# Optimization experiments

Hardware: AMD Instinct MI355X
Metric: run time of the kernel (lower is better)

## Reference

```python
import jax, jax.numpy as jnp
import numpy as np

B, N = 8192, 200  # batch of patches, fixed 200 points per patch


def setup_inputs() -> dict:
    key = jax.random.key(0)
    k1, = jax.random.split(key, 1)
    network_in = jax.random.normal(k1, (B, N, 13), dtype=jnp.float32)
    # learned parameters per build(): outward_shift init 0.25, a init 1, b init 0
    outward_shift = jnp.full((1,), 0.25, dtype=jnp.float32)
    a = jnp.ones((1,), dtype=jnp.float32)
    b = jnp.zeros((1,), dtype=jnp.float32)
    return {"network_in": network_in, "outward_shift": outward_shift, "a": a, "b": b}


def reference(network_in, outward_shift, a, b):
    w = network_in[:, :, 0:1]          # [B,N,1]
    xyz1 = network_in[:, :, 1:4]
    xyz2 = network_in[:, :, 4:7]       # also orig_xyz2
    norm1 = network_in[:, :, 7:10]
    norm2 = network_in[:, :, 10:13]

    w = jax.nn.relu(a * w + b) + 1e-8  # [B,N,1]

    v1 = xyz1 + norm1 * outward_shift
    v2 = xyz2 + norm2 * outward_shift

    w_sum = jnp.sum(w, axis=1)                       # [B,1]
    v1_ctr = jnp.sum(v1 * w, axis=1) / w_sum         # [B,3]
    v2_ctr = jnp.sum(v2 * w, axis=1) / w_sum         # [B,3]
    v1 = v1 - v1_ctr[:, None, :]
    v2 = v2 - v2_ctr[:, None, :]

    # cov = v2^T diag(w) v1, done without materializing the NxN diagonal
    cov = jnp.einsum('bni,bn,bnj->bij', v2, w[:, :, 0], v1)  # [B,3,3]

    # tf.linalg.svd: cov = u diag(s) v^T  ->  jnp svd: cov = u diag(s) vh, v = vh^T
    u, s, vh = jnp.linalg.svd(cov)
    v = jnp.swapaxes(vh, -1, -2)

    VUt = jnp.einsum('bik,bjk->bij', v, u)           # v @ u^T
    det_VUt = jnp.linalg.det(VUt)                    # [B]
    ones = jnp.ones_like(det_VUt)
    d = jnp.stack([ones, ones, det_VUt], axis=-1)    # [B,3]

    # R = v @ diag([1,1,det]) @ u^T
    R = jnp.einsum('bik,bk,bjk->bij', v, d, u)       # [B,3,3]

    t = v1_ctr - jnp.einsum('bij,bj->bi', R, v2_ctr) # [B,3]
    new_coords = jnp.einsum('bij,bnj->bni', R, xyz2) + t[:, None, :]
    return new_coords
```

## Files before the change

### kernel.cpp

```cpp
#include <hip/hip_runtime.h>
#include <math.h>

#define NPTS 200
#define NCH  13
#define BLK  256
#define FPB  (NPTS * NCH)
#define STG  2560

typedef float f4u __attribute__((ext_vector_type(4), aligned(4)));

typedef struct { float x, y, z; } f3s;

#define ACCUMULATE(Q0,Q1,Q2,Q3,Q4,Q5,Q6,Q7,Q8,Q9,Q10,Q11,Q12)               \
    {                                                                        \
        float wt = aa * (Q0) + bb;                                           \
        wt = fmaxf(wt, 0.f) + 1e-8f;                                         \
        const float v1x = fmaf(shift, (Q7),  (Q1));                          \
        const float v1y = fmaf(shift, (Q8),  (Q2));                          \
        const float v1z = fmaf(shift, (Q9),  (Q3));                          \
        const float v2x = fmaf(shift, (Q10), (Q4));                          \
        const float v2y = fmaf(shift, (Q11), (Q5));                          \
        const float v2z = fmaf(shift, (Q12), (Q6));                          \
        const float wv2x = wt * v2x, wv2y = wt * v2y, wv2z = wt * v2z;       \
        acc[0] += wt;                                                        \
        acc[1] += wt * v1x; acc[2] += wt * v1y; acc[3] += wt * v1z;          \
        acc[4] += wv2x;     acc[5] += wv2y;     acc[6] += wv2z;              \
        acc[7]  += wv2x * v1x; acc[8]  += wv2x * v1y; acc[9]  += wv2x * v1z; \
        acc[10] += wv2y * v1x; acc[11] += wv2y * v1y; acc[12] += wv2y * v1z; \
        acc[13] += wv2z * v1x; acc[14] += wv2z * v1y; acc[15] += wv2z * v1z; \
    }

__global__ __launch_bounds__(BLK, 4) void fused_kernel(
    const float* __restrict__ net_in,
    const float* __restrict__ shift_p,
    const float* __restrict__ a_p,
    const float* __restrict__ b_p,
    float* __restrict__ out)
{
    __shared__ float s_in[4 * STG];

    const int tid = threadIdx.x;
    const int w   = tid >> 6;
    const int l   = tid & 63;
    const int b   = blockIdx.x * 4 + w;

    const float shift = shift_p[0];
    const float aa    = a_p[0];
    const float bb    = b_p[0];

    const float* src = net_in + (size_t)b * FPB;
    float*       dst = s_in + w * STG;

    #pragma unroll
    for (int j = 0; j < 10; ++j) {
        __builtin_amdgcn_global_load_lds(
            (const __attribute__((address_space(1))) void*)(src + j * 256 + l * 4),
            (__attribute__((address_space(3))) void*)(dst + j * 256),
            16, 0, 0);
    }

    f4u t0v = {0.f, 0.f, 0.f, 0.f};
    f4u t1v = {0.f, 0.f, 0.f, 0.f};
    f4u t2v = {0.f, 0.f, 0.f, 0.f};
    float t12 = 0.f;
    if (l < 8) {
        const float* tp = src + (192 + l) * NCH;
        t0v = *(const f4u*)(tp);
        t1v = *(const f4u*)(tp + 4);
        t2v = *(const f4u*)(tp + 8);
        t12 = tp[12];
    }

    __builtin_amdgcn_s_waitcnt(0);
    __asm__ __volatile__("" ::: "memory");

    float acc[16];
    #pragma unroll
    for (int k = 0; k < 16; ++k) acc[k] = 0.f;

    float sx2[4], sy2[4], sz2[4];

    #pragma unroll
    for (int j = 0; j < 3; ++j) {
        const int p = l + 64 * j;
        const float* q = dst + p * NCH;
        const float q0 = q[0],  q1 = q[1],  q2  = q[2],  q3  = q[3];
        const float q4 = q[4],  q5 = q[5],  q6  = q[6],  q7  = q[7];
        const float q8 = q[8],  q9 = q[9],  q10 = q[10], q11 = q[11], q12 = q[12];
        ACCUMULATE(q0, q1, q2, q3, q4, q5, q6, q7, q8, q9, q10, q11, q12)
        sx2[j] = q4; sy2[j] = q5; sz2[j] = q6;
    }
    sx2[3] = t1v.x; sy2[3] = t1v.y; sz2[3] = t1v.z;
    if (l < 8) {
        ACCUMULATE(t0v.x, t0v.y, t0v.z, t0v.w,
                   t1v.x, t1v.y, t1v.z, t1v.w,
                   t2v.x, t2v.y, t2v.z, t2v.w, t12)
    }

    #pragma unroll
    for (int k = 0; k < 16; ++k) {
        acc[k] += __shfl_xor(acc[k], 32, 64);
        acc[k] += __shfl_xor(acc[k], 16, 64);
        acc[k] += __shfl_xor(acc[k],  8, 64);
        acc[k] += __shfl_xor(acc[k],  4, 64);
        acc[k] += __shfl_xor(acc[k],  2, 64);
        acc[k] += __shfl_xor(acc[k],  1, 64);
    }

    const float W = acc[0];
    const float invW = 1.0f / W;
    const float v1cx = acc[1] * invW, v1cy = acc[2] * invW, v1cz = acc[3] * invW;
    const float v2cx = acc[4] * invW, v2cy = acc[5] * invW, v2cz = acc[6] * invW;

    const float Sxx = acc[7]  - W * v2cx * v1cx;
    const float Sxy = acc[8]  - W * v2cx * v1cy;
    const float Sxz = acc[9]  - W * v2cx * v1cz;
    const float Syx = acc[10] - W * v2cy * v1cx;
    const float Syy = acc[11] - W * v2cy * v1cy;
    const float Syz = acc[12] - W * v2cy * v1cz;
    const float Szx = acc[13] - W * v2cz * v1cx;
    const float Szy = acc[14] - W * v2cz * v1cy;
    const float Szz = acc[15] - W * v2cz * v1cz;

    float Am[4][4];
    Am[0][0] = Sxx + Syy + Szz;
    Am[0][1] = Syz - Szy;  Am[0][2] = Szx - Sxz;  Am[0][3] = Sxy - Syx;
    Am[1][1] = Sxx - Syy - Szz;
    Am[1][2] = Sxy + Syx;  Am[1][3] = Szx + Sxz;
    Am[2][2] = -Sxx + Syy - Szz;
    Am[2][3] = Syz + Szy;
    Am[3][3] = -Sxx - Syy + Szz;
    Am[1][0] = Am[0][1]; Am[2][0] = Am[0][2]; Am[3][0] = Am[0][3];
    Am[2][1] = Am[1][2]; Am[3][1] = Am[1][3]; Am[3][2] = Am[2][3];

    float Vm[4][4] = {{1,0,0,0},{0,1,0,0},{0,0,1,0},{0,0,0,1}};

    const int prs[6][2] = {{0,1},{0,2},{0,3},{1,2},{1,3},{2,3}};
    for (int sweep = 0; sweep < 5; ++sweep) {
        #pragma unroll
        for (int r = 0; r < 6; ++r) {
            const int p = prs[r][0], q = prs[r][1];
            float apq = Am[p][q];
            if (apq != 0.0f) {
                float tau = (Am[q][q] - Am[p][p]) / (2.0f * apq);
                float t = copysignf(1.0f, tau) /
                          (fabsf(tau) + sqrtf(1.0f + tau * tau));
                float c = rsqrtf(1.0f + t * t);
                float s = t * c;
                #pragma unroll
                for (int k = 0; k < 4; ++k) {
                    float a1 = Am[p][k], a2 = Am[q][k];
                    Am[p][k] = c * a1 - s * a2;
                    Am[q][k] = s * a1 + c * a2;
                }
                #pragma unroll
                for (int k = 0; k < 4; ++k) {
                    float a1 = Am[k][p], a2 = Am[k][q];
                    Am[k][p] = c * a1 - s * a2;
                    Am[k][q] = s * a1 + c * a2;
                }
                #pragma unroll
                for (int k = 0; k < 4; ++k) {
                    float a1 = Vm[k][p], a2 = Vm[k][q];
                    Vm[k][p] = c * a1 - s * a2;
                    Vm[k][q] = s * a1 + c * a2;
                }
            }
        }
    }

    float bd = Am[0][0];
    float q0 = Vm[0][0], qx = Vm[1][0], qy = Vm[2][0], qz = Vm[3][0];
    if (Am[1][1] > bd) { bd = Am[1][1]; q0 = Vm[0][1]; qx = Vm[1][1]; qy = Vm[2][1]; qz = Vm[3][1]; }
    if (Am[2][2] > bd) { bd = Am[2][2]; q0 = Vm[0][2]; qx = Vm[1][2]; qy = Vm[2][2]; qz = Vm[3][2]; }
    if (Am[3][3] > bd) { bd = Am[3][3]; q0 = Vm[0][3]; qx = Vm[1][3]; qy = Vm[2][3]; qz = Vm[3][3]; }

    const float R00 = q0*q0 + qx*qx - qy*qy - qz*qz;
    const float R01 = 2.0f * (qx*qy - q0*qz);
    const float R02 = 2.0f * (qx*qz + q0*qy);
    const float R10 = 2.0f * (qx*qy + q0*qz);
    const float R11 = q0*q0 - qx*qx + qy*qy - qz*qz;
    const float R12 = 2.0f * (qy*qz - q0*qx);
    const float R20 = 2.0f * (qx*qz - q0*qy);
    const float R21 = 2.0f * (qy*qz + q0*qx);
    const float R22 = q0*q0 - qx*qx - qy*qy + qz*qz;

    const float tx = v1cx - (R00 * v2cx + R01 * v2cy + R02 * v2cz);
    const float ty = v1cy - (R10 * v2cx + R11 * v2cy + R12 * v2cz);
    const float tz = v1cz - (R20 * v2cx + R21 * v2cy + R22 * v2cz);

    float* ob = out + (size_t)b * (NPTS * 3);
    #pragma unroll
    for (int j = 0; j < 4; ++j) {
        if (j < 3 || l < 8) {
            const int p = l + 64 * j;
            const float X = sx2[j], Y = sy2[j], Z = sz2[j];
            f3s o3;
            o3.x = R00 * X + R01 * Y + R02 * Z + tx;
            o3.y = R10 * X + R11 * Y + R12 * Z + ty;
            o3.z = R20 * X + R21 * Y + R22 * Z + tz;
            *(f3s*)(ob + p * 3) = o3;
        }
    }
}

extern "C" void kernel_launch(void* const* d_in, const int* in_sizes, int n_in,
                              void* d_out, int out_size, void* d_ws, size_t ws_size,
                              hipStream_t stream) {
    const float* net_in  = (const float*)d_in[0];
    const float* shift_p = (const float*)d_in[1];
    const float* a_p     = (const float*)d_in[2];
    const float* b_p     = (const float*)d_in[3];
    float* out = (float*)d_out;

    const int B = in_sizes[0] / FPB;
    (void)d_ws; (void)ws_size; (void)n_in; (void)out_size;

    fused_kernel<<<B / 4, BLK, 0, stream>>>(net_in, shift_p, a_p, b_p, out);
}
```

Measured before the change: 162.5 us.

## Load points directly from global, reduce via LDS, solve eigenproblem in one thread per patch

Drops the global-to-LDS staging and reads each point's 13 channels straight from global memory with vector loads. The 16 accumulators are now reduced with two shuffles plus an LDS transpose-sum instead of six xor-shuffle rounds. The 4x4 Jacobi eigen solve runs in only 4 threads per block, one per patch, rather than redundantly in all 64 lanes, and it uses fast rcp/sqrt/rsq intrinsics plus quaternion renormalisation. Risks: uncoalesced 13-float-stride global loads, two block barriers, and a serial tail where only 4 lanes are active.

```diff
diff --git a/kernel.cpp b/kernel.cpp
--- a/kernel.cpp
+++ b/kernel.cpp
@@ -5,7 +5,6 @@
 #define NCH  13
 #define BLK  256
 #define FPB  (NPTS * NCH)
-#define STG  2560
 
 typedef float f4u __attribute__((ext_vector_type(4), aligned(4)));
 
@@ -37,7 +36,9 @@
     const float* __restrict__ b_p,
     float* __restrict__ out)
 {
-    __shared__ float s_in[4 * STG];
+    __shared__ float s_part[4][16][20];
+    __shared__ float s_sums[4][16];
+    __shared__ float s_Rt[4][12];
 
     const int tid = threadIdx.x;
     const int w   = tid >> 6;
@@ -49,30 +50,6 @@
     const float bb    = b_p[0];
 
     const float* src = net_in + (size_t)b * FPB;
-    float*       dst = s_in + w * STG;
-
-    #pragma unroll
-    for (int j = 0; j < 10; ++j) {
-        __builtin_amdgcn_global_load_lds(
-            (const __attribute__((address_space(1))) void*)(src + j * 256 + l * 4),
-            (__attribute__((address_space(3))) void*)(dst + j * 256),
-            16, 0, 0);
-    }
-
-    f4u t0v = {0.f, 0.f, 0.f, 0.f};
-    f4u t1v = {0.f, 0.f, 0.f, 0.f};
-    f4u t2v = {0.f, 0.f, 0.f, 0.f};
-    float t12 = 0.f;
-    if (l < 8) {
-        const float* tp = src + (192 + l) * NCH;
-        t0v = *(const f4u*)(tp);
-        t1v = *(const f4u*)(tp + 4);
-        t2v = *(const f4u*)(tp + 8);
-        t12 = tp[12];
-    }
-
-    __builtin_amdgcn_s_waitcnt(0);
-    __asm__ __volatile__("" ::: "memory");
 
     float acc[16];
     #pragma unroll
@@ -81,113 +58,142 @@
     float sx2[4], sy2[4], sz2[4];
 
     #pragma unroll
-    for (int j = 0; j < 3; ++j) {
-        const int p = l + 64 * j;
-        const float* q = dst + p * NCH;
-        const float q0 = q[0],  q1 = q[1],  q2  = q[2],  q3  = q[3];
-        const float q4 = q[4],  q5 = q[5],  q6  = q[6],  q7  = q[7];
-        const float q8 = q[8],  q9 = q[9],  q10 = q[10], q11 = q[11], q12 = q[12];
-        ACCUMULATE(q0, q1, q2, q3, q4, q5, q6, q7, q8, q9, q10, q11, q12)
-        sx2[j] = q4; sy2[j] = q5; sz2[j] = q6;
-    }
-    sx2[3] = t1v.x; sy2[3] = t1v.y; sz2[3] = t1v.z;
-    if (l < 8) {
-        ACCUMULATE(t0v.x, t0v.y, t0v.z, t0v.w,
-                   t1v.x, t1v.y, t1v.z, t1v.w,
-                   t2v.x, t2v.y, t2v.z, t2v.w, t12)
+    for (int j = 0; j < 4; ++j) {
+        if (j < 3 || l < 8) {
+            const float* q = src + (l + 64 * j) * NCH;
+            const f4u v0 = *(const f4u*)(q);
+            const f4u v1 = *(const f4u*)(q + 4);
+            const f4u v2 = *(const f4u*)(q + 8);
+            const float q12 = q[12];
+            ACCUMULATE(v0.x, v0.y, v0.z, v0.w,
+                       v1.x, v1.y, v1.z, v1.w,
+                       v2.x, v2.y, v2.z, v2.w, q12)
+            sx2[j] = v1.x; sy2[j] = v1.y; sz2[j] = v1.z;
+        } else {
+            sx2[j] = 0.f; sy2[j] = 0.f; sz2[j] = 0.f;
+        }
     }
 
     #pragma unroll
     for (int k = 0; k < 16; ++k) {
-        acc[k] += __shfl_xor(acc[k], 32, 64);
-        acc[k] += __shfl_xor(acc[k], 16, 64);
-        acc[k] += __shfl_xor(acc[k],  8, 64);
-        acc[k] += __shfl_xor(acc[k],  4, 64);
-        acc[k] += __shfl_xor(acc[k],  2, 64);
-        acc[k] += __shfl_xor(acc[k],  1, 64);
-    }
-
-    const float W = acc[0];
-    const float invW = 1.0f / W;
-    const float v1cx = acc[1] * invW, v1cy = acc[2] * invW, v1cz = acc[3] * invW;
-    const float v2cx = acc[4] * invW, v2cy = acc[5] * invW, v2cz = acc[6] * invW;
-
-    const float Sxx = acc[7]  - W * v2cx * v1cx;
-    const float Sxy = acc[8]  - W * v2cx * v1cy;
-    const float Sxz = acc[9]  - W * v2cx * v1cz;
-    const float Syx = acc[10] - W * v2cy * v1cx;
-    const float Syy = acc[11] - W * v2cy * v1cy;
-    const float Syz = acc[12] - W * v2cy * v1cz;
-    const float Szx = acc[13] - W * v2cz * v1cx;
-    const float Szy = acc[14] - W * v2cz * v1cy;
-    const float Szz = acc[15] - W * v2cz * v1cz;
-
-    float Am[4][4];
-    Am[0][0] = Sxx + Syy + Szz;
-    Am[0][1] = Syz - Szy;  Am[0][2] = Szx - Sxz;  Am[0][3] = Sxy - Syx;
-    Am[1][1] = Sxx - Syy - Szz;
-    Am[1][2] = Sxy + Syx;  Am[1][3] = Szx + Sxz;
-    Am[2][2] = -Sxx + Syy - Szz;
-    Am[2][3] = Syz + Szy;
-    Am[3][3] = -Sxx - Syy + Szz;
-    Am[1][0] = Am[0][1]; Am[2][0] = Am[0][2]; Am[3][0] = Am[0][3];
-    Am[2][1] = Am[1][2]; Am[3][1] = Am[1][3]; Am[3][2] = Am[2][3];
-
-    float Vm[4][4] = {{1,0,0,0},{0,1,0,0},{0,0,1,0},{0,0,0,1}};
-
-    const int prs[6][2] = {{0,1},{0,2},{0,3},{1,2},{1,3},{2,3}};
-    for (int sweep = 0; sweep < 5; ++sweep) {
+        acc[k] += __shfl_down(acc[k], 32, 64);
+        acc[k] += __shfl_down(acc[k], 16, 64);
+    }
+    if (l < 16) {
+        float4* pp = (float4*)&s_part[w][l][0];
+        pp[0] = make_float4(acc[0],  acc[1],  acc[2],  acc[3]);
+        pp[1] = make_float4(acc[4],  acc[5],  acc[6],  acc[7]);
+        pp[2] = make_float4(acc[8],  acc[9],  acc[10], acc[11]);
+        pp[3] = make_float4(acc[12], acc[13], acc[14], acc[15]);
+        float s = 0.f;
         #pragma unroll
-        for (int r = 0; r < 6; ++r) {
-            const int p = prs[r][0], q = prs[r][1];
-            float apq = Am[p][q];
-            if (apq != 0.0f) {
-                float tau = (Am[q][q] - Am[p][p]) / (2.0f * apq);
-                float t = copysignf(1.0f, tau) /
-                          (fabsf(tau) + sqrtf(1.0f + tau * tau));
-                float c = rsqrtf(1.0f + t * t);
-                float s = t * c;
-                #pragma unroll
-                for (int k = 0; k < 4; ++k) {
-                    float a1 = Am[p][k], a2 = Am[q][k];
-                    Am[p][k] = c * a1 - s * a2;
-                    Am[q][k] = s * a1 + c * a2;
-                }
-                #pragma unroll
-                for (int k = 0; k < 4; ++k) {
-                    float a1 = Am[k][p], a2 = Am[k][q];
-                    Am[k][p] = c * a1 - s * a2;
-                    Am[k][q] = s * a1 + c * a2;
-                }
-                #pragma unroll
-                for (int k = 0; k < 4; ++k) {
-                    float a1 = Vm[k][p], a2 = Vm[k][q];
-                    Vm[k][p] = c * a1 - s * a2;
-                    Vm[k][q] = s * a1 + c * a2;
+        for (int r = 0; r < 16; ++r) s += s_part[w][r][l];
+        s_sums[w][l] = s;
+    }
+    __syncthreads();
+
+    if (tid < 4) {
+        float f[16];
+        #pragma unroll
+        for (int k = 0; k < 16; ++k) f[k] = s_sums[tid][k];
+
+        const float W = f[0];
+        const float invW = __builtin_amdgcn_rcpf(W);
+        const float v1cx = f[1] * invW, v1cy = f[2] * invW, v1cz = f[3] * invW;
+        const float v2cx = f[4] * invW, v2cy = f[5] * invW, v2cz = f[6] * invW;
+
+        const float Sxx = f[7]  - W * v2cx * v1cx;
+        const float Sxy = f[8]  - W * v2cx * v1cy;
+        const float Sxz = f[9]  - W * v2cx * v1cz;
+        const float Syx = f[10] - W * v2cy * v1cx;
+        const float Syy = f[11] - W * v2cy * v1cy;
+        const float Syz = f[12] - W * v2cy * v1cz;
+        const float Szx = f[13] - W * v2cz * v1cx;
+        const float Szy = f[14] - W * v2cz * v1cy;
+        const float Szz = f[15] - W * v2cz * v1cz;
+
+        float Am[4][4];
+        Am[0][0] = Sxx + Syy + Szz;
+        Am[0][1] = Syz - Szy;  Am[0][2] = Szx - Sxz;  Am[0][3] = Sxy - Syx;
+        Am[1][1] = Sxx - Syy - Szz;
+        Am[1][2] = Sxy + Syx;  Am[1][3] = Szx + Sxz;
+        Am[2][2] = -Sxx + Syy - Szz;
+        Am[2][3] = Syz + Szy;
+        Am[3][3] = -Sxx - Syy + Szz;
+        Am[1][0] = Am[0][1]; Am[2][0] = Am[0][2]; Am[3][0] = Am[0][3];
+        Am[2][1] = Am[1][2]; Am[3][1] = Am[1][3]; Am[3][2] = Am[2][3];
+
+        float Vm[4][4] = {{1,0,0,0},{0,1,0,0},{0,0,1,0},{0,0,0,1}};
+
+        const int prs[6][2] = {{0,1},{0,2},{0,3},{1,2},{1,3},{2,3}};
+        for (int sweep = 0; sweep < 5; ++sweep) {
+            #pragma unroll
+            for (int r = 0; r < 6; ++r) {
+                const int p = prs[r][0], q = prs[r][1];
+                float apq = Am[p][q];
+                if (apq != 0.0f) {
+                    float tau = (Am[q][q] - Am[p][p]) * 0.5f *
+                                __builtin_amdgcn_rcpf(apq);
+                    float t = copysignf(1.0f, tau) * __builtin_amdgcn_rcpf(
+                                fabsf(tau) +
+                                __builtin_amdgcn_sqrtf(fmaf(tau, tau, 1.0f)));
+                    float c = __builtin_amdgcn_rsqf(fmaf(t, t, 1.0f));
+                    float s = t * c;
+                    #pragma unroll
+                    for (int k = 0; k < 4; ++k) {
+                        float a1 = Am[p][k], a2 = Am[q][k];
+                        Am[p][k] = c * a1 - s * a2;
+                        Am[q][k] = s * a1 + c * a2;
+                    }
+                    #pragma unroll
+                    for (int k = 0; k < 4; ++k) {
+                        float a1 = Am[k][p], a2 = Am[k][q];
+                        Am[k][p] = c * a1 - s * a2;
+                        Am[k][q] = s * a1 + c * a2;
+                    }
+                    #pragma unroll
+                    for (int k = 0; k < 4; ++k) {
+                        float a1 = Vm[k][p], a2 = Vm[k][q];
+                        Vm[k][p] = c * a1 - s * a2;
+                        Vm[k][q] = s * a1 + c * a2;
+                    }
                 }
             }
         }
-    }
-
-    float bd = Am[0][0];
-    float q0 = Vm[0][0], qx = Vm[1][0], qy = Vm[2][0], qz = Vm[3][0];
-    if (Am[1][1] > bd) { bd = Am[1][1]; q0 = Vm[0][1]; qx = Vm[1][1]; qy = Vm[2][1]; qz = Vm[3][1]; }
-    if (Am[2][2] > bd) { bd = Am[2][2]; q0 = Vm[0][2]; qx = Vm[1][2]; qy = Vm[2][2]; qz = Vm[3][2]; }
-    if (Am[3][3] > bd) { bd = Am[3][3]; q0 = Vm[0][3]; qx = Vm[1][3]; qy = Vm[2][3]; qz = Vm[3][3]; }
-
-    const float R00 = q0*q0 + qx*qx - qy*qy - qz*qz;
-    const float R01 = 2.0f * (qx*qy - q0*qz);
-    const float R02 = 2.0f * (qx*qz + q0*qy);
-    const float R10 = 2.0f * (qx*qy + q0*qz);
-    const float R11 = q0*q0 - qx*qx + qy*qy - qz*qz;
-    const float R12 = 2.0f * (qy*qz - q0*qx);
-    const float R20 = 2.0f * (qx*qz - q0*qy);
-    const float R21 = 2.0f * (qy*qz + q0*qx);
-    const float R22 = q0*q0 - qx*qx - qy*qy + qz*qz;
-
-    const float tx = v1cx - (R00 * v2cx + R01 * v2cy + R02 * v2cz);
-    const float ty = v1cy - (R10 * v2cx + R11 * v2cy + R12 * v2cz);
-    const float tz = v1cz - (R20 * v2cx + R21 * v2cy + R22 * v2cz);
+
+        float bd = Am[0][0];
+        float q0 = Vm[0][0], qx = Vm[1][0], qy = Vm[2][0], qz = Vm[3][0];
+        if (Am[1][1] > bd) { bd = Am[1][1]; q0 = Vm[0][1]; qx = Vm[1][1]; qy = Vm[2][1]; qz = Vm[3][1]; }
+        if (Am[2][2] > bd) { bd = Am[2][2]; q0 = Vm[0][2]; qx = Vm[1][2]; qy = Vm[2][2]; qz = Vm[3][2]; }
+        if (Am[3][3] > bd) { bd = Am[3][3]; q0 = Vm[0][3]; qx = Vm[1][3]; qy = Vm[2][3]; qz = Vm[3][3]; }
+
+        const float qn = __builtin_amdgcn_rsqf(q0*q0 + qx*qx + qy*qy + qz*qz);
+        q0 *= qn; qx *= qn; qy *= qn; qz *= qn;
+
+        const float R00 = q0*q0 + qx*qx - qy*qy - qz*qz;
+        const float R01 = 2.0f * (qx*qy - q0*qz);
+        const float R02 = 2.0f * (qx*qz + q0*qy);
+        const float R10 = 2.0f * (qx*qy + q0*qz);
+        const float R11 = q0*q0 - qx*qx + qy*qy - qz*qz;
+        const float R12 = 2.0f * (qy*qz - q0*qx);
+        const float R20 = 2.0f * (qx*qz - q0*qy);
+        const float R21 = 2.0f * (qy*qz + q0*qx);
+        const float R22 = q0*q0 - qx*qx - qy*qy + qz*qz;
+
+        float* o = &s_Rt[tid][0];
+        o[0] = R00; o[1]  = R01; o[2]  = R02;
+        o[3] = R10; o[4]  = R11; o[5]  = R12;
+        o[6] = R20; o[7]  = R21; o[8]  = R22;
+        o[9]  = v1cx - (R00 * v2cx + R01 * v2cy + R02 * v2cz);
+        o[10] = v1cy - (R10 * v2cx + R11 * v2cy + R12 * v2cz);
+        o[11] = v1cz - (R20 * v2cx + R21 * v2cy + R22 * v2cz);
+    }
+    __syncthreads();
+
+    const float R00 = s_Rt[w][0], R01 = s_Rt[w][1],  R02 = s_Rt[w][2];
+    const float R10 = s_Rt[w][3], R11 = s_Rt[w][4],  R12 = s_Rt[w][5];
+    const float R20 = s_Rt[w][6], R21 = s_Rt[w][7],  R22 = s_Rt[w][8];
+    const float tx  = s_Rt[w][9], ty  = s_Rt[w][10], tz  = s_Rt[w][11];
 
     float* ob = out + (size_t)b * (NPTS * 3);
     #pragma unroll
```

Result: faster. 144.4 us (-11.2%).

## Load patch points directly from global memory and use fast hardware reciprocals

Applied to the files above, without the earlier changes.

Drops the LDS staging buffer and its async global-to-LDS copies. Each lane now reads its 13 channels straight from global memory with unaligned float4 loads, which removes the shared-memory footprint and the full waitcnt barrier. The Jacobi rotations and centroid division switch to raw hardware rcp, sqrt and rsq builtins in place of IEEE division. The quaternion is renormalised to compensate for the lower precision. The risk is uncoalesced strided global loads (13-float stride per lane) in exchange for removing LDS traffic and raising occupancy.

```diff
diff --git a/kernel.cpp b/kernel.cpp
--- a/kernel.cpp
+++ b/kernel.cpp
@@ -5,7 +5,6 @@
 #define NCH  13
 #define BLK  256
 #define FPB  (NPTS * NCH)
-#define STG  2560
 
 typedef float f4u __attribute__((ext_vector_type(4), aligned(4)));
 
@@ -37,8 +36,6 @@
     const float* __restrict__ b_p,
     float* __restrict__ out)
 {
-    __shared__ float s_in[4 * STG];
-
     const int tid = threadIdx.x;
     const int w   = tid >> 6;
     const int l   = tid & 63;
@@ -49,30 +46,6 @@
     const float bb    = b_p[0];
 
     const float* src = net_in + (size_t)b * FPB;
-    float*       dst = s_in + w * STG;
-
-    #pragma unroll
-    for (int j = 0; j < 10; ++j) {
-        __builtin_amdgcn_global_load_lds(
-            (const __attribute__((address_space(1))) void*)(src + j * 256 + l * 4),
-            (__attribute__((address_space(3))) void*)(dst + j * 256),
-            16, 0, 0);
-    }
-
-    f4u t0v = {0.f, 0.f, 0.f, 0.f};
-    f4u t1v = {0.f, 0.f, 0.f, 0.f};
-    f4u t2v = {0.f, 0.f, 0.f, 0.f};
-    float t12 = 0.f;
-    if (l < 8) {
-        const float* tp = src + (192 + l) * NCH;
-        t0v = *(const f4u*)(tp);
-        t1v = *(const f4u*)(tp + 4);
-        t2v = *(const f4u*)(tp + 8);
-        t12 = tp[12];
-    }
-
-    __builtin_amdgcn_s_waitcnt(0);
-    __asm__ __volatile__("" ::: "memory");
 
     float acc[16];
     #pragma unroll
@@ -81,20 +54,20 @@
     float sx2[4], sy2[4], sz2[4];
 
     #pragma unroll
-    for (int j = 0; j < 3; ++j) {
-        const int p = l + 64 * j;
-        const float* q = dst + p * NCH;
-        const float q0 = q[0],  q1 = q[1],  q2  = q[2],  q3  = q[3];
-        const float q4 = q[4],  q5 = q[5],  q6  = q[6],  q7  = q[7];
-        const float q8 = q[8],  q9 = q[9],  q10 = q[10], q11 = q[11], q12 = q[12];
-        ACCUMULATE(q0, q1, q2, q3, q4, q5, q6, q7, q8, q9, q10, q11, q12)
-        sx2[j] = q4; sy2[j] = q5; sz2[j] = q6;
-    }
-    sx2[3] = t1v.x; sy2[3] = t1v.y; sz2[3] = t1v.z;
-    if (l < 8) {
-        ACCUMULATE(t0v.x, t0v.y, t0v.z, t0v.w,
-                   t1v.x, t1v.y, t1v.z, t1v.w,
-                   t2v.x, t2v.y, t2v.z, t2v.w, t12)
+    for (int j = 0; j < 4; ++j) {
+        if (j < 3 || l < 8) {
+            const float* q = src + (l + 64 * j) * NCH;
+            const f4u v0 = *(const f4u*)(q);
+            const f4u v1 = *(const f4u*)(q + 4);
+            const f4u v2 = *(const f4u*)(q + 8);
+            const float q12 = q[12];
+            ACCUMULATE(v0.x, v0.y, v0.z, v0.w,
+                       v1.x, v1.y, v1.z, v1.w,
+                       v2.x, v2.y, v2.z, v2.w, q12)
+            sx2[j] = v1.x; sy2[j] = v1.y; sz2[j] = v1.z;
+        } else {
+            sx2[j] = 0.f; sy2[j] = 0.f; sz2[j] = 0.f;
+        }
     }
 
     #pragma unroll
@@ -108,7 +81,7 @@
     }
 
     const float W = acc[0];
-    const float invW = 1.0f / W;
+    const float invW = __builtin_amdgcn_rcpf(W);
     const float v1cx = acc[1] * invW, v1cy = acc[2] * invW, v1cz = acc[3] * invW;
     const float v2cx = acc[4] * invW, v2cy = acc[5] * invW, v2cz = acc[6] * invW;
 
@@ -142,10 +115,12 @@
             const int p = prs[r][0], q = prs[r][1];
             float apq = Am[p][q];
             if (apq != 0.0f) {
-                float tau = (Am[q][q] - Am[p][p]) / (2.0f * apq);
-                float t = copysignf(1.0f, tau) /
-                          (fabsf(tau) + sqrtf(1.0f + tau * tau));
-                float c = rsqrtf(1.0f + t * t);
+                float tau = (Am[q][q] - Am[p][p]) * 0.5f *
+                            __builtin_amdgcn_rcpf(apq);
+                float t = copysignf(1.0f, tau) * __builtin_amdgcn_rcpf(
+                            fabsf(tau) +
+                            __builtin_amdgcn_sqrtf(fmaf(tau, tau, 1.0f)));
+                float c = __builtin_amdgcn_rsqf(fmaf(t, t, 1.0f));
                 float s = t * c;
                 #pragma unroll
                 for (int k = 0; k < 4; ++k) {
@@ -174,6 +149,9 @@
     if (Am[1][1] > bd) { bd = Am[1][1]; q0 = Vm[0][1]; qx = Vm[1][1]; qy = Vm[2][1]; qz = Vm[3][1]; }
     if (Am[2][2] > bd) { bd = Am[2][2]; q0 = Vm[0][2]; qx = Vm[1][2]; qy = Vm[2][2]; qz = Vm[3][2]; }
     if (Am[3][3] > bd) { bd = Am[3][3]; q0 = Vm[0][3]; qx = Vm[1][3]; qy = Vm[2][3]; qz = Vm[3][3]; }
+
+    const float qn = __builtin_amdgcn_rsqf(q0*q0 + qx*qx + qy*qy + qz*qz);
+    q0 *= qn; qx *= qn; qy *= qn; qz *= qn;
 
     const float R00 = q0*q0 + qx*qx - qy*qy - qz*qz;
     const float R01 = 2.0f * (qx*qy - q0*qz);
```

Measured after the change: 154.4 us. 5.0% less time.

## Streamline 4x4 Jacobi eigensolver with scalar symmetric entries and fast intrinsics

Applied to the files above, without the earlier changes.

Replaces the full 4x4 array Jacobi rotation with a symmetric scalar form. Each rotation updates the two diagonal entries in closed form, zeroes the pivot, and rotates only the four affected off-diagonal entries. Divisions and square roots become hardware rcp/sqrt/rsq intrinsics, and the sweep count drops from five to four, with a quaternion renormalisation added afterwards. This cuts per-thread ALU work and register pressure in the serial eigen-solve tail, at the cost of lower-precision intrinsics and one fewer sweep, which could affect accuracy.

```diff
diff --git a/kernel.cpp b/kernel.cpp
--- a/kernel.cpp
+++ b/kernel.cpp
@@ -30,6 +30,32 @@
         acc[13] += wv2z * v1x; acc[14] += wv2z * v1y; acc[15] += wv2z * v1z; \
     }
 
+#define ROT(dp, dq, opq, e1p, e1q, e2p, e2q, P, Q)                           \
+    {                                                                        \
+        const float apq = opq;                                               \
+        if (apq != 0.0f) {                          \
+            const float tau = (dq - dp) * 0.5f * __builtin_amdgcn_rcpf(apq); \
+            const float tt  = copysignf(1.0f, tau) * __builtin_amdgcn_rcpf(  \
+                                fabsf(tau) +                                 \
+                                __builtin_amdgcn_sqrtf(fmaf(tau, tau, 1.0f)));\
+            const float c = __builtin_amdgcn_rsqf(fmaf(tt, tt, 1.0f));       \
+            const float s = tt * c;                                          \
+            dp -= tt * apq;                                                  \
+            dq += tt * apq;                                                  \
+            opq = 0.0f;                                                      \
+            { const float t1 = e1p; e1p = c * t1 - s * e1q;                  \
+              e1q = s * t1 + c * e1q; }                                      \
+            { const float t2 = e2p; e2p = c * t2 - s * e2q;                  \
+              e2q = s * t2 + c * e2q; }                                      \
+            _Pragma("unroll")                                                \
+            for (int k = 0; k < 4; ++k) {                                    \
+                const float a1 = Vm[k][P], a2 = Vm[k][Q];                    \
+                Vm[k][P] = c * a1 - s * a2;                                  \
+                Vm[k][Q] = s * a1 + c * a2;                                  \
+            }                                                                \
+        }                                                                    \
+    }
+
 __global__ __launch_bounds__(BLK, 4) void fused_kernel(
     const float* __restrict__ net_in,
     const float* __restrict__ shift_p,
@@ -52,10 +78,10 @@
     float*       dst = s_in + w * STG;
 
     #pragma unroll
-    for (int j = 0; j < 10; ++j) {
+    for (int jj = 0; jj < 10; ++jj) {
         __builtin_amdgcn_global_load_lds(
-            (const __attribute__((address_space(1))) void*)(src + j * 256 + l * 4),
-            (__attribute__((address_space(3))) void*)(dst + j * 256),
+            (const __attribute__((address_space(1))) void*)(src + jj * 256 + l * 4),
+            (__attribute__((address_space(3))) void*)(dst + jj * 256),
             16, 0, 0);
     }
 
@@ -81,14 +107,14 @@
     float sx2[4], sy2[4], sz2[4];
 
     #pragma unroll
-    for (int j = 0; j < 3; ++j) {
-        const int p = l + 64 * j;
+    for (int jj = 0; jj < 3; ++jj) {
+        const int p = l + 64 * jj;
         const float* q = dst + p * NCH;
         const float q0 = q[0],  q1 = q[1],  q2  = q[2],  q3  = q[3];
         const float q4 = q[4],  q5 = q[5],  q6  = q[6],  q7  = q[7];
         const float q8 = q[8],  q9 = q[9],  q10 = q[10], q11 = q[11], q12 = q[12];
         ACCUMULATE(q0, q1, q2, q3, q4, q5, q6, q7, q8, q9, q10, q11, q12)
-        sx2[j] = q4; sy2[j] = q5; sz2[j] = q6;
+        sx2[jj] = q4; sy2[jj] = q5; sz2[jj] = q6;
     }
     sx2[3] = t1v.x; sy2[3] = t1v.y; sz2[3] = t1v.z;
     if (l < 8) {
@@ -108,7 +134,7 @@
     }
 
     const float W = acc[0];
-    const float invW = 1.0f / W;
+    const float invW = __builtin_amdgcn_rcpf(W);
     const float v1cx = acc[1] * invW, v1cy = acc[2] * invW, v1cz = acc[3] * invW;
     const float v2cx = acc[4] * invW, v2cy = acc[5] * invW, v2cz = acc[6] * invW;
 
@@ -122,58 +148,36 @@
     const float Szy = acc[14] - W * v2cz * v1cy;
     const float Szz = acc[15] - W * v2cz * v1cz;
 
-    float Am[4][4];
-    Am[0][0] = Sxx + Syy + Szz;
-    Am[0][1] = Syz - Szy;  Am[0][2] = Szx - Sxz;  Am[0][3] = Sxy - Syx;
-    Am[1][1] = Sxx - Syy - Szz;
-    Am[1][2] = Sxy + Syx;  Am[1][3] = Szx + Sxz;
-    Am[2][2] = -Sxx + Syy - Szz;
-    Am[2][3] = Syz + Szy;
-    Am[3][3] = -Sxx - Syy + Szz;
-    Am[1][0] = Am[0][1]; Am[2][0] = Am[0][2]; Am[3][0] = Am[0][3];
-    Am[2][1] = Am[1][2]; Am[3][1] = Am[1][3]; Am[3][2] = Am[2][3];
+    float d0  = Sxx + Syy + Szz;
+    float o01 = Syz - Szy;
+    float o02 = Szx - Sxz;
+    float o03 = Sxy - Syx;
+    float d1  = Sxx - Syy - Szz;
+    float o12 = Sxy + Syx;
+    float o13 = Szx + Sxz;
+    float d2  = -Sxx + Syy - Szz;
+    float o23 = Syz + Szy;
+    float d3  = -Sxx - Syy + Szz;
 
     float Vm[4][4] = {{1,0,0,0},{0,1,0,0},{0,0,1,0},{0,0,0,1}};
 
-    const int prs[6][2] = {{0,1},{0,2},{0,3},{1,2},{1,3},{2,3}};
-    for (int sweep = 0; sweep < 5; ++sweep) {
-        #pragma unroll
-        for (int r = 0; r < 6; ++r) {
-            const int p = prs[r][0], q = prs[r][1];
-            float apq = Am[p][q];
-            if (apq != 0.0f) {
-                float tau = (Am[q][q] - Am[p][p]) / (2.0f * apq);
-                float t = copysignf(1.0f, tau) /
-                          (fabsf(tau) + sqrtf(1.0f + tau * tau));
-                float c = rsqrtf(1.0f + t * t);
-                float s = t * c;
-                #pragma unroll
-                for (int k = 0; k < 4; ++k) {
-                    float a1 = Am[p][k], a2 = Am[q][k];
-                    Am[p][k] = c * a1 - s * a2;
-                    Am[q][k] = s * a1 + c * a2;
-                }
-                #pragma unroll
-                for (int k = 0; k < 4; ++k) {
-                    float a1 = Am[k][p], a2 = Am[k][q];
-                    Am[k][p] = c * a1 - s * a2;
-                    Am[k][q] = s * a1 + c * a2;
-                }
-                #pragma unroll
-                for (int k = 0; k < 4; ++k) {
-                    float a1 = Vm[k][p], a2 = Vm[k][q];
-                    Vm[k][p] = c * a1 - s * a2;
-                    Vm[k][q] = s * a1 + c * a2;
-                }
-            }
-        }
-    }
-
-    float bd = Am[0][0];
+    for (int sweep = 0; sweep < 4; ++sweep) {
+        ROT(d0, d1, o01,  o02, o12,  o03, o13,  0, 1)
+        ROT(d0, d2, o02,  o01, o12,  o03, o23,  0, 2)
+        ROT(d0, d3, o03,  o01, o13,  o02, o23,  0, 3)
+        ROT(d1, d2, o12,  o01, o02,  o13, o23,  1, 2)
+        ROT(d1, d3, o13,  o01, o03,  o12, o23,  1, 3)
+        ROT(d2, d3, o23,  o02, o03,  o12, o13,  2, 3)
+    }
+
+    float bd = d0;
     float q0 = Vm[0][0], qx = Vm[1][0], qy = Vm[2][0], qz = Vm[3][0];
-    if (Am[1][1] > bd) { bd = Am[1][1]; q0 = Vm[0][1]; qx = Vm[1][1]; qy = Vm[2][1]; qz = Vm[3][1]; }
-    if (Am[2][2] > bd) { bd = Am[2][2]; q0 = Vm[0][2]; qx = Vm[1][2]; qy = Vm[2][2]; qz = Vm[3][2]; }
-    if (Am[3][3] > bd) { bd = Am[3][3]; q0 = Vm[0][3]; qx = Vm[1][3]; qy = Vm[2][3]; qz = Vm[3][3]; }
+    if (d1 > bd) { bd = d1; q0 = Vm[0][1]; qx = Vm[1][1]; qy = Vm[2][1]; qz = Vm[3][1]; }
+    if (d2 > bd) { bd = d2; q0 = Vm[0][2]; qx = Vm[1][2]; qy = Vm[2][2]; qz = Vm[3][2]; }
+    if (d3 > bd) { bd = d3; q0 = Vm[0][3]; qx = Vm[1][3]; qy = Vm[2][3]; qz = Vm[3][3]; }
+
+    const float qn = __builtin_amdgcn_rsqf(q0*q0 + qx*qx + qy*qy + qz*qz);
+    q0 *= qn; qx *= qn; qy *= qn; qz *= qn;
 
     const float R00 = q0*q0 + qx*qx - qy*qy - qz*qz;
     const float R01 = 2.0f * (qx*qy - q0*qz);
@@ -191,10 +195,10 @@
 
     float* ob = out + (size_t)b * (NPTS * 3);
     #pragma unroll
-    for (int j = 0; j < 4; ++j) {
-        if (j < 3 || l < 8) {
-            const int p = l + 64 * j;
-            const float X = sx2[j], Y = sy2[j], Z = sz2[j];
+    for (int jj = 0; jj < 4; ++jj) {
+        if (jj < 3 || l < 8) {
+            const int p = l + 64 * jj;
+            const float X = sx2[jj], Y = sy2[jj], Z = sz2[jj];
             f3s o3;
             o3.x = R00 * X + R01 * Y + R02 * Z + tx;
             o3.y = R10 * X + R11 * Y + R12 * Z + ty;
```

Measured after the change: 159.2 us. 1.02x faster.
